# Optimization experiments

Measured on AMD Instinct MI355X. Metric: run time of the kernel, lower is better.

The kernel has to match this reference:

```python
import jax, jax.numpy as jnp
import numpy as np

NUM_NODES = 20000
NUM_EDGES = 320000
NODE_DIM = 256
EDGE_DIM = 64
HIDDEN = 512

def _glorot(key, shape):
    fan_in = shape[0]
    bound = 1.0 / np.sqrt(fan_in)
    return jax.random.uniform(key, shape, jnp.float32, -bound, bound)

def setup_inputs() -> dict:
    key = jax.random.key(0)
    ks = jax.random.split(key, 12)
    node_features = jax.random.normal(ks[0], (NUM_NODES, NODE_DIM), jnp.float32)
    edge_index = jax.random.randint(ks[1], (2, NUM_EDGES), 0, NUM_NODES, jnp.int64 if jax.config.jax_enable_x64 else jnp.int32)
    edge_features = jax.random.normal(ks[2], (NUM_EDGES, EDGE_DIM), jnp.float32)
    edge_in = 2 * NODE_DIM + EDGE_DIM
    node_in = NODE_DIM + HIDDEN
    params = {
        'W1': _glorot(ks[3], (edge_in, HIDDEN)), 'b1': _glorot(ks[4], (HIDDEN,)),
        'W2': _glorot(ks[5], (HIDDEN, HIDDEN)), 'b2': _glorot(ks[6], (HIDDEN,)),
        'W3': _glorot(ks[7], (node_in, HIDDEN)), 'b3': _glorot(ks[8], (HIDDEN,)),
        'W4': _glorot(ks[9], (HIDDEN, NODE_DIM)), 'b4': _glorot(ks[10], (NODE_DIM,)),
    }
    return {'node_features': node_features, 'edge_index': edge_index,
            'edge_features': edge_features, **params}

def reference(node_features, edge_index, edge_features,
              W1, b1, W2, b2, W3, b3, W4, b4):
    src_idx = edge_index[0]
    tgt_idx = edge_index[1]
    # gather endpoints: [E, 2*node_dim + edge_dim]
    edge_input = jnp.concatenate(
        [node_features[src_idx], node_features[tgt_idx], edge_features], axis=-1)
    # edge MLP
    h = jax.nn.relu(edge_input @ W1 + b1)
    messages = h @ W2 + b2                      # [E, hidden]
    # scatter-add aggregate per target node
    aggregated = jax.ops.segment_sum(messages, tgt_idx, num_segments=NUM_NODES)
    # node MLP + residual
    node_input = jnp.concatenate([node_features, aggregated], axis=-1)
    g = jax.nn.relu(node_input @ W3 + b3)
    node_update = g @ W4 + b4                   # [N, node_dim]
    return node_features + node_update
```

## Files before the change

kernel.cpp:

```cpp
#include <hip/hip_runtime.h>

#define NUM_NODES 20000
#define NUM_EDGES 320000
#define NODE_DIM  256
#define EDGE_DIM  64
#define HIDDEN    512

typedef short  s16x8  __attribute__((ext_vector_type(8)));
typedef float  f32x16 __attribute__((ext_vector_type(16)));
typedef unsigned short us16;

__device__ __forceinline__ us16 f2bf(float f) {
    union { float f; unsigned u; } c; c.f = f;
    unsigned r = c.u + 0x7fffu + ((c.u >> 16) & 1u);
    return (us16)(r >> 16);
}
__device__ __forceinline__ float bf2f(us16 b) {
    union { unsigned u; float f; } c; c.u = ((unsigned)b) << 16;
    return c.f;
}
__device__ __forceinline__ int swapmid(int x) {
    return (x & 3) | ((x & 4) << 1) | ((x & 8) >> 1);
}
__device__ __forceinline__ void zero16(f32x16& a) {
    #pragma unroll
    for (int i = 0; i < 16; ++i) a[i] = 0.0f;
}
__device__ __forceinline__ void mfma3(f32x16& acc, s16x8 ah, s16x8 al, s16x8 bh, s16x8 bl) {
    acc = __builtin_amdgcn_mfma_f32_32x32x16_bf16(ah, bh, acc, 0, 0, 0);
    acc = __builtin_amdgcn_mfma_f32_32x32x16_bf16(ah, bl, acc, 0, 0, 0);
    acc = __builtin_amdgcn_mfma_f32_32x32x16_bf16(al, bh, acc, 0, 0, 0);
}
template<int STRIDE>
__device__ __forceinline__ void stash_quad(char* hi, char* lo, int r, int c, float4 v) {
    int cpp = (c & ~15) | swapmid(c & 15);
    int off = r * STRIDE + ((cpp * 2) ^ ((r & 7) << 4));
    us16 h0 = f2bf(v.x), h1 = f2bf(v.y), h2 = f2bf(v.z), h3 = f2bf(v.w);
    uint2 uh; uh.x = h0 | ((unsigned)h1 << 16); uh.y = h2 | ((unsigned)h3 << 16);
    uint2 ul;
    ul.x = f2bf(v.x - bf2f(h0)) | ((unsigned)f2bf(v.y - bf2f(h1)) << 16);
    ul.y = f2bf(v.z - bf2f(h2)) | ((unsigned)f2bf(v.w - bf2f(h3)) << 16);
    *reinterpret_cast<uint2*>(hi + off) = uh;
    *reinterpret_cast<uint2*>(lo + off) = ul;
}
template<int STRIDE>
__device__ __forceinline__ void bread(const char* hi, const char* lo, int r, int kbyte,
                                      s16x8& bh, s16x8& bl) {
    int off = r * STRIDE + (kbyte ^ ((r & 7) << 4));
    bh = *reinterpret_cast<const s16x8*>(hi + off);
    bl = *reinterpret_cast<const s16x8*>(lo + off);
}

__global__ void build_deg(const int* __restrict__ tgt, int* __restrict__ deg) {
    int i = blockIdx.x * 256 + threadIdx.x;
    if (i < NUM_EDGES) atomicAdd(&deg[tgt[i]], 1);
}

__global__ void scan_deg(const int* __restrict__ deg, int* __restrict__ off) {
    __shared__ int sums[1024];
    const int tid  = threadIdx.x;
    const int base = tid * 20;
    int local[20];
    int s = 0;
    #pragma unroll
    for (int i = 0; i < 20; ++i) {
        local[i] = s;
        int idx = base + i;
        s += (idx < NUM_NODES) ? deg[idx] : 0;
    }
    sums[tid] = s;
    __syncthreads();
    for (int d = 1; d < 1024; d <<= 1) {
        int add = (tid >= d) ? sums[tid - d] : 0;
        __syncthreads();
        sums[tid] += add;
        __syncthreads();
    }
    const int chunk_off = sums[tid] - s;
    #pragma unroll
    for (int i = 0; i < 20; ++i) {
        int idx = base + i;
        if (idx <= NUM_NODES) off[idx] = chunk_off + local[i];
    }
}

__global__ void fill_csr(const int* __restrict__ tgt, const int* __restrict__ off,
                         int* __restrict__ cursor, int* __restrict__ csr) {
    int i = blockIdx.x * 256 + threadIdx.x;
    if (i < NUM_EDGES) {
        int t = tgt[i];
        int p = atomicAdd(&cursor[t], 1);
        csr[off[t] + p] = i;
    }
}

__global__ void compute_w23(const float* __restrict__ W2, const float* __restrict__ b2,
                            const float* __restrict__ W3,
                            float* __restrict__ W23, float* __restrict__ b23) {
    int n = blockIdx.y * 256 + threadIdx.x;
    int i = blockIdx.x;
    const float* w3b = W3 + 256 * 512 + n;
    float s = 0.f;
    if (i < 512) {
        const float* w2r = W2 + i * 512;
        for (int j = 0; j < 512; ++j) s = fmaf(w2r[j], w3b[(size_t)j * 512], s);
        W23[i * 512 + n] = s;
    } else {
        for (int j = 0; j < 512; ++j) s = fmaf(b2[j], w3b[(size_t)j * 512], s);
        b23[n] = s;
    }
}

__global__ void prep_planes(const float* __restrict__ W1, const float* __restrict__ W3,
                            const float* __restrict__ W4, const float* __restrict__ W23,
                            us16* __restrict__ wab_h, us16* __restrict__ wab_l,
                            us16* __restrict__ wc_h,  us16* __restrict__ wc_l,
                            us16* __restrict__ w34_h, us16* __restrict__ w34_l,
                            us16* __restrict__ w4_h,  us16* __restrict__ w4_l) {
    int idx = blockIdx.x * 256 + threadIdx.x;
    float w; us16 *dh, *dl; int k, n, N;
    if (idx < 262144) {
        n = idx & 1023; k = idx >> 10; N = 1024;
        w = W1[(k + (n >= 512 ? 256 : 0)) * 512 + (n & 511)];
        dh = wab_h; dl = wab_l;
    } else if (idx < 294912) {
        int j = idx - 262144; n = j & 511; k = j >> 9; N = 512;
        w = W1[(512 + k) * 512 + n];
        dh = wc_h; dl = wc_l;
    } else if (idx < 688128) {
        int j = idx - 294912; n = j & 511; k = j >> 9; N = 512;
        w = (k < 256) ? W3[k * 512 + n] : W23[(k - 256) * 512 + n];
        dh = w34_h; dl = w34_l;
    } else {
        int j = idx - 688128; n = j & 255; k = j >> 8; N = 256;
        w = W4[k * 256 + n];
        dh = w4_h; dl = w4_l;
    }
    us16 h = f2bf(w);
    us16 l = f2bf(w - bf2f(h));
    int d = (k >> 4) * (N * 16) + n * 16 + swapmid(k & 15);
    dh[d] = h; dl[d] = l;
}

__global__ __launch_bounds__(512, 2)
void gemm_p(const float* __restrict__ nf,
            const us16* __restrict__ wab_h, const us16* __restrict__ wab_l,
            float* __restrict__ P) {
    extern __shared__ char sB[];
    const int tid = threadIdx.x;
    const int nb  = blockIdx.x * 64;
    const int half = blockIdx.y;

    const float4* nf4 = reinterpret_cast<const float4*>(nf);
    for (int i = tid; i < 64 * 64; i += 512) {
        int r = i >> 6, q = i & 63;
        int row = nb + r; if (row >= NUM_NODES) row = NUM_NODES - 1;
        stash_quad<512>(sB, sB + 32768, r, 4 * q, nf4[(size_t)row * 64 + q]);
    }
    __syncthreads();

    const int w = tid >> 6, l = tid & 63, le = l & 31, g = l >> 5;
    const s16x8* Ah = reinterpret_cast<const s16x8*>(wab_h);
    const s16x8* Al = reinterpret_cast<const s16x8*>(wab_l);
    const int nbase = half * 512 + w * 64;

    f32x16 acc[2][2];
    #pragma unroll
    for (int a = 0; a < 2; ++a) { zero16(acc[a][0]); zero16(acc[a][1]); }

    for (int ks = 0; ks < 16; ++ks) {
        s16x8 AH[2], AL[2], bh[2], bl[2];
        #pragma unroll
        for (int mt = 0; mt < 2; ++mt) {
            int idx = ks * 2048 + (nbase + 32 * mt + le) * 2 + g;
            AH[mt] = Ah[idx]; AL[mt] = Al[idx];
        }
        #pragma unroll
        for (int rt = 0; rt < 2; ++rt)
            bread<512>(sB, sB + 32768, 32 * rt + le, ks * 32 + 16 * g, bh[rt], bl[rt]);
        #pragma unroll
        for (int mt = 0; mt < 2; ++mt)
            #pragma unroll
            for (int rt = 0; rt < 2; ++rt)
                mfma3(acc[mt][rt], AH[mt], AL[mt], bh[rt], bl[rt]);
    }

    float4* P4 = reinterpret_cast<float4*>(P);
    #pragma unroll
    for (int rt = 0; rt < 2; ++rt) {
        int row = nb + 32 * rt + le;
        if (row < NUM_NODES) {
            #pragma unroll
            for (int mt = 0; mt < 2; ++mt)
                #pragma unroll
                for (int rq = 0; rq < 4; ++rq) {
                    int nn = nbase + 32 * mt + 4 * g + 8 * rq;
                    float4 o = make_float4(acc[mt][rt][4*rq+0], acc[mt][rt][4*rq+1],
                                           acc[mt][rt][4*rq+2], acc[mt][rt][4*rq+3]);
                    P4[(size_t)row * 256 + (nn >> 2)] = o;
                }
        }
    }
}

__global__ __launch_bounds__(512, 4)
void edge_csr(const int* __restrict__ srcI, const int* __restrict__ tgtI,
              const int* __restrict__ csr, const float* __restrict__ ef,
              const us16* __restrict__ wc_h, const us16* __restrict__ wc_l,
              const float* __restrict__ b1, const float* __restrict__ P,
              float* __restrict__ aggH) {
    extern __shared__ char dsm[];
    char* sC = dsm;
    char* sB = dsm + 65536;
    __shared__ int sEid[64], sSrc[64], sTgt[64];

    const int tid  = threadIdx.x;
    const int orig = blockIdx.x;
    const int wg   = (orig & 7) * 625 + (orig >> 3);
    const int cb   = wg * 64;

    if (tid < 64) {
        int eid = csr[cb + tid];
        sEid[tid] = eid; sSrc[tid] = srcI[eid]; sTgt[tid] = tgtI[eid];
    }
    __syncthreads();

    const float4* ef4 = reinterpret_cast<const float4*>(ef);
    const float4* P4  = reinterpret_cast<const float4*>(P);
    const float4* b14 = reinterpret_cast<const float4*>(b1);
    const int w = tid >> 6, l = tid & 63, le = l & 31, g = l >> 5;
    const int grp = tid >> 7, slice = tid & 127;
    const s16x8* Ah = reinterpret_cast<const s16x8*>(wc_h);
    const s16x8* Al = reinterpret_cast<const s16x8*>(wc_l);

    #pragma unroll
    for (int half = 0; half < 2; ++half) {
        const int e0 = half * 32 + grp * 8;
        {
            const int se = tid >> 4, sq = tid & 15;
            stash_quad<128>(sB, sB + 4096, se, 4 * sq,
                            ef4[(size_t)sEid[half * 32 + se] * 16 + sq]);
        }
        __syncthreads();

        #pragma unroll
        for (int mt = 0; mt < 2; ++mt) {
            f32x16 acc; zero16(acc);
            #pragma unroll
            for (int ks = 0; ks < 4; ++ks) {
                int idx = ks * 1024 + (w * 64 + 32 * mt + le) * 2 + g;
                s16x8 bh, bl;
                bread<128>(sB, sB + 4096, le, ks * 32 + 16 * g, bh, bl);
                mfma3(acc, Ah[idx], Al[idx], bh, bl);
            }
            #pragma unroll
            for (int rq = 0; rq < 4; ++rq) {
                int h0 = w * 64 + 32 * mt + 4 * g + 8 * rq;
                float4 bq = b14[h0 >> 2];
                float4 v = make_float4(acc[4*rq+0] + bq.x, acc[4*rq+1] + bq.y,
                                       acc[4*rq+2] + bq.z, acc[4*rq+3] + bq.w);
                *reinterpret_cast<float4*>(sC + le * 2048 + ((h0 * 4) ^ ((le & 15) << 4))) = v;
            }
        }
        __syncthreads();

        {
            float4 pa[8];
            #pragma unroll
            for (int i = 0; i < 8; ++i)
                pa[i] = P4[(size_t)sSrc[e0 + i] * 256 + slice];
            int tcur = sTgt[e0];
            float4 pt = P4[(size_t)tcur * 256 + 128 + slice];
            float4 sum = make_float4(0.f, 0.f, 0.f, 0.f);
            #pragma unroll
            for (int i = 0; i < 8; ++i) {
                int eg = e0 + i;
                int t = sTgt[eg];
                if (t != tcur) {
                    float* d = aggH + (size_t)tcur * 512 + slice * 4;
                    atomicAdd(d + 0, sum.x); atomicAdd(d + 1, sum.y);
                    atomicAdd(d + 2, sum.z); atomicAdd(d + 3, sum.w);
                    sum = make_float4(0.f, 0.f, 0.f, 0.f);
                    tcur = t;
                    pt = P4[(size_t)t * 256 + 128 + slice];
                }
                int crow = eg & 31;
                float4 c = *reinterpret_cast<const float4*>(
                    sC + crow * 2048 + ((slice * 16) ^ ((crow & 15) << 4)));
                sum.x += fmaxf(pa[i].x + pt.x + c.x, 0.f);
                sum.y += fmaxf(pa[i].y + pt.y + c.y, 0.f);
                sum.z += fmaxf(pa[i].z + pt.z + c.z, 0.f);
                sum.w += fmaxf(pa[i].w + pt.w + c.w, 0.f);
            }
            float* d = aggH + (size_t)tcur * 512 + slice * 4;
            atomicAdd(d + 0, sum.x); atomicAdd(d + 1, sum.y);
            atomicAdd(d + 2, sum.z); atomicAdd(d + 3, sum.w);
        }
        __syncthreads();
    }
}

__global__ __launch_bounds__(512, 2)
void node_mlp(const float* __restrict__ nf, const float* __restrict__ aggH,
              const int* __restrict__ deg,
              const us16* __restrict__ w34_h, const us16* __restrict__ w34_l,
              const us16* __restrict__ w4_h,  const us16* __restrict__ w4_l,
              const float* __restrict__ b3, const float* __restrict__ b23,
              const float* __restrict__ b4, float* __restrict__ out) {
    extern __shared__ char sm[];
    __shared__ int sDeg[32];
    const int tid = threadIdx.x;
    const int nb  = blockIdx.x * 32;

    if (tid < 32) sDeg[tid] = deg[nb + tid];

    const float4* nf4 = reinterpret_cast<const float4*>(nf);
    const float4* ag4 = reinterpret_cast<const float4*>(aggH);
    auto stage = [&](int c, char* buf) {
        for (int i = tid; i < 32 * 64; i += 512) {
            int r = i >> 6, q = i & 63;
            float4 v = (c == 0) ? nf4[(size_t)(nb + r) * 64 + q]
                                : ag4[(size_t)(nb + r) * 128 + (c - 1) * 64 + q];
            stash_quad<512>(buf, buf + 16384, r, 4 * q, v);
        }
    };

    stage(0, sm);
    __syncthreads();

    const int w = tid >> 6, l = tid & 63, le = l & 31, g = l >> 5;

    f32x16 acc[2]; zero16(acc[0]); zero16(acc[1]);
    {
        const s16x8* Ah = reinterpret_cast<const s16x8*>(w34_h);
        const s16x8* Al = reinterpret_cast<const s16x8*>(w34_l);
        #pragma unroll
        for (int c = 0; c < 3; ++c) {
            char* cur = sm + (c & 1) * 32768;
            char* oth = sm + ((c + 1) & 1) * 32768;
            if (c < 2) stage(c + 1, oth);
            #pragma unroll
            for (int ksl = 0; ksl < 16; ++ksl) {
                int ks = c * 16 + ksl;
                s16x8 AH[2], AL[2], bh, bl;
                #pragma unroll
                for (int mt = 0; mt < 2; ++mt) {
                    int idx = ks * 1024 + (w * 64 + 32 * mt + le) * 2 + g;
                    AH[mt] = Ah[idx]; AL[mt] = Al[idx];
                }
                bread<512>(cur, cur + 16384, le, ksl * 32 + 16 * g, bh, bl);
                #pragma unroll
                for (int mt = 0; mt < 2; ++mt) mfma3(acc[mt], AH[mt], AL[mt], bh, bl);
            }
            __syncthreads();
        }
    }

    {
        const float4* b34  = reinterpret_cast<const float4*>(b3);
        const float4* b234 = reinterpret_cast<const float4*>(b23);
        const float degv = (float)sDeg[le];
        #pragma unroll
        for (int mt = 0; mt < 2; ++mt)
            #pragma unroll
            for (int rq = 0; rq < 4; ++rq) {
                int hcol = w * 64 + 32 * mt + 4 * g + 8 * rq;
                float4 bq = b34[hcol >> 2], cq = b234[hcol >> 2];
                float4 gv;
                gv.x = fmaxf(acc[mt][4*rq+0] + bq.x + degv * cq.x, 0.f);
                gv.y = fmaxf(acc[mt][4*rq+1] + bq.y + degv * cq.y, 0.f);
                gv.z = fmaxf(acc[mt][4*rq+2] + bq.z + degv * cq.z, 0.f);
                gv.w = fmaxf(acc[mt][4*rq+3] + bq.w + degv * cq.w, 0.f);
                stash_quad<1024>(sm, sm + 32768, le, hcol, gv);
            }
    }
    __syncthreads();

    f32x16 a2; zero16(a2);
    {
        const s16x8* Ah = reinterpret_cast<const s16x8*>(w4_h);
        const s16x8* Al = reinterpret_cast<const s16x8*>(w4_l);
        for (int ks = 0; ks < 32; ++ks) {
            s16x8 AH, AL, bh, bl;
            int idx = ks * 512 + (w * 32 + le) * 2 + g;
            AH = Ah[idx]; AL = Al[idx];
            bread<1024>(sm, sm + 32768, le, ks * 32 + 16 * g, bh, bl);
            mfma3(a2, AH, AL, bh, bl);
        }
    }

    const float4* b44 = reinterpret_cast<const float4*>(b4);
    float4* out4 = reinterpret_cast<float4*>(out);
    #pragma unroll
    for (int rq = 0; rq < 4; ++rq) {
        int n0 = w * 32 + 4 * g + 8 * rq;
        float4 bq  = b44[n0 >> 2];
        float4 res = nf4[(size_t)(nb + le) * 64 + (n0 >> 2)];
        float4 o;
        o.x = res.x + a2[4*rq+0] + bq.x;
        o.y = res.y + a2[4*rq+1] + bq.y;
        o.z = res.z + a2[4*rq+2] + bq.z;
        o.w = res.w + a2[4*rq+3] + bq.w;
        out4[(size_t)(nb + le) * 64 + (n0 >> 2)] = o;
    }
}

extern "C" void kernel_launch(void* const* d_in, const int* in_sizes, int n_in,
                              void* d_out, int out_size, void* d_ws, size_t ws_size,
                              hipStream_t stream) {
    const float* nf = (const float*)d_in[0];
    const int*   ei = (const int*)d_in[1];
    const float* ef = (const float*)d_in[2];
    const float* W1 = (const float*)d_in[3];
    const float* b1 = (const float*)d_in[4];
    const float* W2 = (const float*)d_in[5];
    const float* b2 = (const float*)d_in[6];
    const float* W3 = (const float*)d_in[7];
    const float* b3 = (const float*)d_in[8];
    const float* W4 = (const float*)d_in[9];
    const float* b4 = (const float*)d_in[10];
    float* out = (float*)d_out;

    char* ws = (char*)d_ws;
    float* P      = (float*)(ws + 0);
    float* aggH   = (float*)(ws + 81920000);
    us16*  wab_h  = (us16*)(ws + 122880000);
    us16*  wab_l  = (us16*)(ws + 123404288);
    us16*  wc_h   = (us16*)(ws + 123928576);
    us16*  wc_l   = (us16*)(ws + 123994112);
    us16*  w34_h  = (us16*)(ws + 124059648);
    us16*  w34_l  = (us16*)(ws + 124846080);
    us16*  w4_h   = (us16*)(ws + 125632512);
    us16*  w4_l   = (us16*)(ws + 125894656);
    float* W23    = (float*)(ws + 126156800);
    float* b23    = (float*)(ws + 127205376);
    int*   deg    = (int*)  (ws + 127207424);
    int*   cursor = (int*)  (ws + 127287424);
    int*   offs   = (int*)  (ws + 127367424);
    int*   csr    = (int*)  (ws + 127447440);

    const int* src = ei;
    const int* tgt = ei + NUM_EDGES;

    (void)hipFuncSetAttribute(reinterpret_cast<const void*>(&edge_csr),
                              hipFuncAttributeMaxDynamicSharedMemorySize, 73728);
    (void)hipFuncSetAttribute(reinterpret_cast<const void*>(&node_mlp),
                              hipFuncAttributeMaxDynamicSharedMemorySize, 65536);
    (void)hipFuncSetAttribute(reinterpret_cast<const void*>(&gemm_p),
                              hipFuncAttributeMaxDynamicSharedMemorySize, 65536);

    hipMemsetAsync(deg, 0, 160000, stream);
    hipMemsetAsync(aggH, 0, (size_t)NUM_NODES * HIDDEN * 4, stream);

    build_deg<<<1250, 256, 0, stream>>>(tgt, deg);
    scan_deg<<<1, 1024, 0, stream>>>(deg, offs);
    fill_csr<<<1250, 256, 0, stream>>>(tgt, offs, cursor, csr);

    compute_w23<<<dim3(513, 2), 256, 0, stream>>>(W2, b2, W3, W23, b23);
    prep_planes<<<3200, 256, 0, stream>>>(W1, W3, W4, W23,
                                          wab_h, wab_l, wc_h, wc_l,
                                          w34_h, w34_l, w4_h, w4_l);

    gemm_p<<<dim3(313, 2), 512, 65536, stream>>>(nf, wab_h, wab_l, P);
    edge_csr<<<5000, 512, 73728, stream>>>(src, tgt, csr, ef, wc_h, wc_l, b1, P, aggH);
    node_mlp<<<625, 512, 65536, stream>>>(nf, aggH, deg, w34_h, w34_l,
                                          w4_h, w4_l, b3, b23, b4, out);
}
```

Measured before the change: 807.8 us.

## Assign target nodes to edge blocks and drop atomics and aggregate memset

New measurement: 931.0 us. +15.3%, slower.

```diff
diff --git a/kernel.cpp b/kernel.cpp
--- a/kernel.cpp
+++ b/kernel.cpp
@@ -84,13 +84,14 @@
     }
 }
 
-__global__ void fill_csr(const int* __restrict__ tgt, const int* __restrict__ off,
-                         int* __restrict__ cursor, int* __restrict__ csr) {
+__global__ void fill_csr(const int* __restrict__ src, const int* __restrict__ tgt,
+                         const int* __restrict__ off,
+                         int* __restrict__ cursor, int2* __restrict__ csr2) {
     int i = blockIdx.x * 256 + threadIdx.x;
     if (i < NUM_EDGES) {
         int t = tgt[i];
         int p = atomicAdd(&cursor[t], 1);
-        csr[off[t] + p] = i;
+        csr2[off[t] + p] = make_int2(i, src[i]);
     }
 }
 
@@ -204,42 +205,50 @@
 }
 
 __global__ __launch_bounds__(512, 4)
-void edge_csr(const int* __restrict__ srcI, const int* __restrict__ tgtI,
-              const int* __restrict__ csr, const float* __restrict__ ef,
+void edge_csr(const int2* __restrict__ csr2, const int* __restrict__ offs,
+              const float* __restrict__ ef,
               const us16* __restrict__ wc_h, const us16* __restrict__ wc_l,
               const float* __restrict__ b1, const float* __restrict__ P,
               float* __restrict__ aggH) {
     extern __shared__ char dsm[];
     char* sC = dsm;
     char* sB = dsm + 65536;
-    __shared__ int sEid[64], sSrc[64], sTgt[64];
+    __shared__ int sOff[5];
 
     const int tid  = threadIdx.x;
     const int orig = blockIdx.x;
     const int wg   = (orig & 7) * 625 + (orig >> 3);
-    const int cb   = wg * 64;
-
-    if (tid < 64) {
-        int eid = csr[cb + tid];
-        sEid[tid] = eid; sSrc[tid] = srcI[eid]; sTgt[tid] = tgtI[eid];
-    }
+    const int t0   = wg * 4;
+
+    if (tid < 5) sOff[tid] = offs[t0 + tid];
     __syncthreads();
+
+    const int ebase = sOff[0];
+    const int eend  = sOff[4];
+    const int L     = eend - ebase;
+    const int nwin  = (L + 31) >> 5;
 
     const float4* ef4 = reinterpret_cast<const float4*>(ef);
     const float4* P4  = reinterpret_cast<const float4*>(P);
     const float4* b14 = reinterpret_cast<const float4*>(b1);
     const int w = tid >> 6, l = tid & 63, le = l & 31, g = l >> 5;
     const int grp = tid >> 7, slice = tid & 127;
+    const int tg  = t0 + grp;
+    const int tlo = sOff[grp], thi = sOff[grp + 1];
     const s16x8* Ah = reinterpret_cast<const s16x8*>(wc_h);
     const s16x8* Al = reinterpret_cast<const s16x8*>(wc_l);
 
-    #pragma unroll
-    for (int half = 0; half < 2; ++half) {
-        const int e0 = half * 32 + grp * 8;
+    const float4 pt = P4[(size_t)tg * 256 + 128 + slice];
+    float4 sum = make_float4(0.f, 0.f, 0.f, 0.f);
+
+    for (int win = 0; win < nwin; ++win) {
+        const int wbase = ebase + (win << 5);
         {
             const int se = tid >> 4, sq = tid & 15;
-            stash_quad<128>(sB, sB + 4096, se, 4 * sq,
-                            ef4[(size_t)sEid[half * 32 + se] * 16 + sq]);
+            int p  = wbase + se;
+            int pc = (p < eend) ? p : ebase;
+            int eid = csr2[pc].x;
+            stash_quad<128>(sB, sB + 4096, se, 4 * sq, ef4[(size_t)eid * 16 + sq]);
         }
         __syncthreads();
 
@@ -265,39 +274,36 @@
         __syncthreads();
 
         {
-            float4 pa[8];
-            #pragma unroll
-            for (int i = 0; i < 8; ++i)
-                pa[i] = P4[(size_t)sSrc[e0 + i] * 256 + slice];
-            int tcur = sTgt[e0];
-            float4 pt = P4[(size_t)tcur * 256 + 128 + slice];
-            float4 sum = make_float4(0.f, 0.f, 0.f, 0.f);
-            #pragma unroll
-            for (int i = 0; i < 8; ++i) {
-                int eg = e0 + i;
-                int t = sTgt[eg];
-                if (t != tcur) {
-                    float* d = aggH + (size_t)tcur * 512 + slice * 4;
-                    atomicAdd(d + 0, sum.x); atomicAdd(d + 1, sum.y);
-                    atomicAdd(d + 2, sum.z); atomicAdd(d + 3, sum.w);
-                    sum = make_float4(0.f, 0.f, 0.f, 0.f);
-                    tcur = t;
-                    pt = P4[(size_t)t * 256 + 128 + slice];
+            const int lo = (tlo > wbase) ? tlo : wbase;
+            const int hi = (thi < wbase + 32) ? thi : (wbase + 32);
+            for (int base = lo; base < hi; base += 8) {
+                const int m = (hi - base < 8) ? (hi - base) : 8;
+                int srcv[8];
+                #pragma unroll
+                for (int j = 0; j < 8; ++j)
+                    srcv[j] = csr2[base + ((j < m) ? j : 0)].y;
+                float4 pa[8];
+                #pragma unroll
+                for (int j = 0; j < 8; ++j)
+                    pa[j] = P4[(size_t)srcv[j] * 256 + slice];
+                #pragma unroll
+                for (int j = 0; j < 8; ++j) {
+                    if (j < m) {
+                        int crow = (base + j) - wbase;
+                        float4 c = *reinterpret_cast<const float4*>(
+                            sC + crow * 2048 + ((slice * 16) ^ ((crow & 15) << 4)));
+                        sum.x += fmaxf(pa[j].x + pt.x + c.x, 0.f);
+                        sum.y += fmaxf(pa[j].y + pt.y + c.y, 0.f);
+                        sum.z += fmaxf(pa[j].z + pt.z + c.z, 0.f);
+                        sum.w += fmaxf(pa[j].w + pt.w + c.w, 0.f);
+                    }
                 }
-                int crow = eg & 31;
-                float4 c = *reinterpret_cast<const float4*>(
-                    sC + crow * 2048 + ((slice * 16) ^ ((crow & 15) << 4)));
-                sum.x += fmaxf(pa[i].x + pt.x + c.x, 0.f);
-                sum.y += fmaxf(pa[i].y + pt.y + c.y, 0.f);
-                sum.z += fmaxf(pa[i].z + pt.z + c.z, 0.f);
-                sum.w += fmaxf(pa[i].w + pt.w + c.w, 0.f);
             }
-            float* d = aggH + (size_t)tcur * 512 + slice * 4;
-            atomicAdd(d + 0, sum.x); atomicAdd(d + 1, sum.y);
-            atomicAdd(d + 2, sum.z); atomicAdd(d + 3, sum.w);
         }
         __syncthreads();
     }
+
+    *reinterpret_cast<float4*>(aggH + (size_t)tg * 512 + slice * 4) = sum;
 }
 
 __global__ __launch_bounds__(512, 2)
@@ -437,7 +443,7 @@
     int*   deg    = (int*)  (ws + 127207424);
     int*   cursor = (int*)  (ws + 127287424);
     int*   offs   = (int*)  (ws + 127367424);
-    int*   csr    = (int*)  (ws + 127447440);
+    int2*  csr2   = (int2*) (ws + 127447440);
 
     const int* src = ei;
     const int* tgt = ei + NUM_EDGES;
@@ -450,11 +456,10 @@
                               hipFuncAttributeMaxDynamicSharedMemorySize, 65536);
 
     hipMemsetAsync(deg, 0, 160000, stream);
-    hipMemsetAsync(aggH, 0, (size_t)NUM_NODES * HIDDEN * 4, stream);
 
     build_deg<<<1250, 256, 0, stream>>>(tgt, deg);
     scan_deg<<<1, 1024, 0, stream>>>(deg, offs);
-    fill_csr<<<1250, 256, 0, stream>>>(tgt, offs, cursor, csr);
+    fill_csr<<<1250, 256, 0, stream>>>(src, tgt, offs, cursor, csr2);
 
     compute_w23<<<dim3(513, 2), 256, 0, stream>>>(W2, b2, W3, W23, b23);
     prep_planes<<<3200, 256, 0, stream>>>(W1, W3, W4, W23,
@@ -462,7 +467,7 @@
                                           w34_h, w34_l, w4_h, w4_l);
 
     gemm_p<<<dim3(313, 2), 512, 65536, stream>>>(nf, wab_h, wab_l, P);
-    edge_csr<<<5000, 512, 73728, stream>>>(src, tgt, csr, ef, wc_h, wc_l, b1, P, aggH);
+    edge_csr<<<5000, 512, 73728, stream>>>(csr2, offs, ef, wc_h, wc_l, b1, P, aggH);
     node_mlp<<<625, 512, 65536, stream>>>(nf, aggH, deg, w34_h, w34_l,
                                           w4_h, w4_l, b3, b23, b4, out);
 }
```
